# Optimization experiments

Measured on AMD Instinct MI355X. Metric: run time of the kernel, lower is better.

The kernel has to match this reference:

```python
import jax, jax.numpy as jnp
import numpy as np

N_NODES = 100000
N_EDGES = 1600000
IN_DIM, HID_DIM, OUT_DIM = 128, 64, 40


def setup_inputs() -> dict:
    key = jax.random.key(0)
    k1, k2, k3, k4, k5, k6 = jax.random.split(key, 6)
    x = jax.random.normal(k1, (N_NODES, IN_DIM), dtype=jnp.float32)
    edge_index = jax.random.randint(k2, (2, N_EDGES), 0, N_NODES, dtype=jnp.int64)
    W1 = jax.random.normal(k3, (IN_DIM, HID_DIM), dtype=jnp.float32) * 0.05
    b1 = jnp.zeros((HID_DIM,), dtype=jnp.float32)
    W2 = jax.random.normal(k4, (HID_DIM, OUT_DIM), dtype=jnp.float32) * 0.05
    b2 = jnp.zeros((OUT_DIM,), dtype=jnp.float32)
    return {"x": x, "edge_index": edge_index, "W1": W1, "b1": b1, "W2": W2, "b2": b2}


def gcn_conv(x, src, dst, W, b, n_nodes):
    """PyG GCNConv: linear -> symmetric-normalized aggregation (with self loops) -> + bias."""
    h = x @ W                                                # [N, C_out]
    # degree of targets, including the implicit self loop (weight 1 each)
    deg = jax.ops.segment_sum(jnp.ones_like(dst, dtype=h.dtype), dst,
                              num_segments=n_nodes) + 1.0    # [N]
    dinv = jax.lax.rsqrt(deg)                                # deg >= 1, always valid
    norm = dinv[src] * dinv[dst]                             # [E] edge norm coefficients
    msg = h[src] * norm[:, None]                             # [E, C_out] gather + scale
    agg = jax.ops.segment_sum(msg, dst, num_segments=n_nodes)
    # self-loop contribution: norm_ii = dinv_i * dinv_i
    agg = agg + h * (dinv * dinv)[:, None]
    return agg + b


def reference(x, edge_index, W1, b1, W2, b2):
    src, dst = edge_index[0], edge_index[1]  # source_to_target flow (PyG default)
    n = x.shape[0]
    h = gcn_conv(x, src, dst, W1, b1, n)
    h = jax.nn.relu(h)
    # dropout is identity in eval mode (training=False)
    out = gcn_conv(h, src, dst, W2, b2, n)
    return out
```

## Files before the change

kernel.cpp:

```cpp
#include <hip/hip_runtime.h>
#include <math.h>

#define N_NODES 100000
#define N_EDGES 1600000
#define IN_DIM 128
#define HID_DIM 64
#define OUT_DIM 40

#define NPAD 102400

#define BUCKET_SHIFT 7
#define BUCKET_NODES 128
#define N_BUCKETS 782
#define CHUNK 2048
#define N_CHUNKS 784

typedef _Float16 f16;
typedef _Float16 f16x2 __attribute__((ext_vector_type(2)));
typedef _Float16 f16x4 __attribute__((ext_vector_type(4)));
typedef _Float16 f16x8 __attribute__((ext_vector_type(8)));
typedef float f32x4 __attribute__((ext_vector_type(4)));


__global__ __launch_bounds__(256) void hist_kernel(const int* __restrict__ dst,
                                                   int* __restrict__ hist) {
    __shared__ int lh[N_BUCKETS];
    int c = blockIdx.x;
    int t = threadIdx.x;
    for (int b = t; b < N_BUCKETS; b += 256) lh[b] = 0;
    __syncthreads();
    int e0 = c * CHUNK;
    for (int i = t; i < CHUNK; i += 256) {
        int e = e0 + i;
        if (e < N_EDGES) atomicAdd(&lh[dst[e] >> BUCKET_SHIFT], 1);
    }
    __syncthreads();
    for (int b = t; b < N_BUCKETS; b += 256) hist[c * N_BUCKETS + b] = lh[b];
}

__global__ __launch_bounds__(256) void scan_chunks_kernel(const int* __restrict__ hist,
                                                          int* __restrict__ base,
                                                          int* __restrict__ bucketTotal) {
    __shared__ int lds[256];
    int b = blockIdx.x;
    int t = threadIdx.x;
    int v[4];
    int s = 0;
    for (int k = 0; k < 4; ++k) {
        int c = 4 * t + k;
        int cv = (c < N_CHUNKS) ? hist[c * N_BUCKETS + b] : 0;
        v[k] = s;
        s += cv;
    }
    lds[t] = s;
    __syncthreads();
    for (int off = 1; off < 256; off <<= 1) {
        int val = (t >= off) ? lds[t - off] : 0;
        __syncthreads();
        lds[t] += val;
        __syncthreads();
    }
    int excl = (t == 0) ? 0 : lds[t - 1];
    for (int k = 0; k < 4; ++k) {
        int c = 4 * t + k;
        if (c < N_CHUNKS) base[b * N_CHUNKS + c] = excl + v[k];
    }
    if (t == 255) bucketTotal[b] = lds[255];
}

__global__ __launch_bounds__(256) void scan_buckets_kernel(const int* __restrict__ bucketTotal,
                                                           int* __restrict__ bucketBase) {
    __shared__ int lds[256];
    int t = threadIdx.x;
    int v[4];
    int s = 0;
    for (int k = 0; k < 4; ++k) {
        int b = 4 * t + k;
        int cv = (b < N_BUCKETS) ? bucketTotal[b] : 0;
        v[k] = s;
        s += cv;
    }
    lds[t] = s;
    __syncthreads();
    for (int off = 1; off < 256; off <<= 1) {
        int val = (t >= off) ? lds[t - off] : 0;
        __syncthreads();
        lds[t] += val;
        __syncthreads();
    }
    int excl = (t == 0) ? 0 : lds[t - 1];
    for (int k = 0; k < 4; ++k) {
        int b = 4 * t + k;
        if (b < N_BUCKETS) bucketBase[b] = excl + v[k];
    }
}

__global__ __launch_bounds__(256) void scatter_kernel(const int* __restrict__ src,
                                                      const int* __restrict__ dst,
                                                      const int* __restrict__ base,
                                                      const int* __restrict__ bucketBase,
                                                      int* __restrict__ stage) {
    __shared__ int lbase[N_BUCKETS];
    __shared__ int lcnt[N_BUCKETS];
    int bid = blockIdx.x;
    int chunk = (bid & 7) * 98 + (bid >> 3);
    int t = threadIdx.x;
    for (int b = t; b < N_BUCKETS; b += 256) {
        lbase[b] = base[b * N_CHUNKS + chunk] + bucketBase[b];
        lcnt[b] = 0;
    }
    __syncthreads();
    int e0 = chunk * CHUNK;
    for (int i = t; i < CHUNK; i += 256) {
        int e = e0 + i;
        if (e < N_EDGES) {
            int d = dst[e];
            int b = d >> BUCKET_SHIFT;
            int pos = lbase[b] + atomicAdd(&lcnt[b], 1);
            stage[pos] = ((d & (BUCKET_NODES - 1)) << 17) | src[e];
        }
    }
}

__global__ __launch_bounds__(256) void place_kernel(const int* __restrict__ stage,
                                                    const int* __restrict__ bucketBase,
                                                    int* __restrict__ csr,
                                                    int* __restrict__ row_start,
                                                    int* __restrict__ cnt,
                                                    float* __restrict__ dinv) {
    __shared__ int lhist[BUCKET_NODES];
    __shared__ int lscan[BUCKET_NODES];
    __shared__ int lstart[BUCKET_NODES];
    __shared__ int lcur[BUCKET_NODES];
    int b = blockIdx.x;
    int t = threadIdx.x;
    int est = bucketBase[b];
    int een = (b == N_BUCKETS - 1) ? N_EDGES : bucketBase[b + 1];
    if (t < BUCKET_NODES) { lhist[t] = 0; lcur[t] = 0; }
    __syncthreads();
    for (int e = est + t; e < een; e += 256) atomicAdd(&lhist[stage[e] >> 17], 1);
    __syncthreads();
    if (t < BUCKET_NODES) lscan[t] = lhist[t];
    __syncthreads();
    for (int off = 1; off < BUCKET_NODES; off <<= 1) {
        int val = (t >= off && t < BUCKET_NODES) ? lscan[t - off] : 0;
        __syncthreads();
        if (t < BUCKET_NODES) lscan[t] += val;
        __syncthreads();
    }
    if (t < BUCKET_NODES) {
        int myexcl = (t == 0) ? 0 : lscan[t - 1];
        lstart[t] = est + myexcl;
        int node = (b << BUCKET_SHIFT) + t;
        if (node < N_NODES) {
            row_start[node] = est + myexcl;
            cnt[node] = lhist[t];
            dinv[node] = rsqrtf((float)lhist[t] + 1.0f);
        }
    }
    __syncthreads();
    for (int e = est + t; e < een; e += 256) {
        int rec = stage[e];
        int dl = rec >> 17;
        int pos = lstart[dl] + atomicAdd(&lcur[dl], 1);
        csr[pos] = rec & 0x1FFFF;
    }
}

__global__ __launch_bounds__(256) void w1frag_kernel(const float* __restrict__ W1,
                                                     f16* __restrict__ w1f) {
    int g = blockIdx.x * 256 + threadIdx.x;
    int f = g >> 6, L = g & 63;
    int s = f >> 2, c = f & 3;
    int q = L >> 4, n = L & 15;
    f16x8 v;
#pragma unroll
    for (int j = 0; j < 8; ++j) {
        int k = 32 * s + 8 * q + j;
        v[j] = (f16)W1[k * HID_DIM + 16 * c + n];
    }
    *(f16x8*)&w1f[(size_t)g * 8] = v;
}

__global__ __launch_bounds__(256) void gemm1_kernel(const float* __restrict__ x,
                                                    const f16* __restrict__ w1f,
                                                    const float* __restrict__ dinv,
                                                    f16* __restrict__ h1p) {
    __shared__ f16 aT[1088 * 8];
    int t = threadIdx.x;
    int nodeBase = blockIdx.x * 64;
    int L = t & 63;

    const f16x8* w1f8 = (const f16x8*)w1f;
    f16x8 bfrag[16];
#pragma unroll
    for (int f = 0; f < 16; ++f) bfrag[f] = w1f8[f * 64 + L];

#pragma unroll
    for (int i = 0; i < 8; ++i) {
        int idx = i * 256 + t;
        int node = idx >> 5;
        int col4 = idx & 31;
        int gnode = nodeBase + node;
        if (gnode >= N_NODES) gnode = N_NODES - 1;
        float4 v = *(const float4*)&x[(size_t)gnode * IN_DIM + col4 * 4];
        int w = node >> 4, m = node & 15;
        int s = col4 >> 3, q = (col4 >> 1) & 3, j0 = (col4 & 1) * 4;
        f16x4 h;
        h.x = (f16)v.x; h.y = (f16)v.y; h.z = (f16)v.z; h.w = (f16)v.w;
        int idx16 = (w * 4 + s) * 68 + 17 * q + m;
        *(f16x4*)&aT[idx16 * 8 + j0] = h;
    }
    __syncthreads();

    int wv = t >> 6;
    int q = L >> 4, m = L & 15;
    f32x4 acc[4] = {};
#pragma unroll
    for (int s = 0; s < 4; ++s) {
        f16x8 afrag = *(const f16x8*)&aT[((wv * 4 + s) * 68 + 17 * q + m) * 8];
#pragma unroll
        for (int c = 0; c < 4; ++c)
            acc[c] = __builtin_amdgcn_mfma_f32_16x16x32_f16(afrag, bfrag[s * 4 + c], acc[c], 0, 0, 0);
    }

#pragma unroll
    for (int r = 0; r < 4; ++r) {
        int node = nodeBase + 16 * wv + q * 4 + r;
        if (node < N_NODES) {
            float di = dinv[node];
#pragma unroll
            for (int c = 0; c < 4; ++c)
                h1p[(size_t)node * HID_DIM + 16 * c + m] = (f16)(acc[c][r] * di);
        }
    }
}

__global__ __launch_bounds__(256) void agg1_kernel(const f16* __restrict__ h1p,
                                                   const int* __restrict__ csr,
                                                   const int* __restrict__ row_start,
                                                   const int* __restrict__ cnt,
                                                   const float* __restrict__ dinv,
                                                   const float* __restrict__ b1,
                                                   float* __restrict__ z) {
    int node = blockIdx.x * 8 + (threadIdx.x >> 5);
    int lane = threadIdx.x & 31;
    if (node >= N_NODES) return;
    const f16x2* h = (const f16x2*)h1p;
    float2 acc;
    {
        f16x2 sv = h[(size_t)node * 32 + lane];
        acc.x = (float)sv.x;
        acc.y = (float)sv.y;
    }
    int n = cnt[node];
    const int* cp = csr + row_start[node];
    int k = 0;
    if (n >= 4) {
        int i0 = cp[0], i1 = cp[1], i2 = cp[2], i3 = cp[3];
        for (; k + 8 <= n; k += 4) {
            int j0 = cp[k + 4], j1 = cp[k + 5], j2 = cp[k + 6], j3 = cp[k + 7];
            f16x2 f0 = h[(size_t)i0 * 32 + lane];
            f16x2 f1 = h[(size_t)i1 * 32 + lane];
            f16x2 f2 = h[(size_t)i2 * 32 + lane];
            f16x2 f3 = h[(size_t)i3 * 32 + lane];
            acc.x += (float)f0.x + (float)f1.x + (float)f2.x + (float)f3.x;
            acc.y += (float)f0.y + (float)f1.y + (float)f2.y + (float)f3.y;
            i0 = j0; i1 = j1; i2 = j2; i3 = j3;
        }
        {
            f16x2 f0 = h[(size_t)i0 * 32 + lane];
            f16x2 f1 = h[(size_t)i1 * 32 + lane];
            f16x2 f2 = h[(size_t)i2 * 32 + lane];
            f16x2 f3 = h[(size_t)i3 * 32 + lane];
            acc.x += (float)f0.x + (float)f1.x + (float)f2.x + (float)f3.x;
            acc.y += (float)f0.y + (float)f1.y + (float)f2.y + (float)f3.y;
            k += 4;
        }
    }
    for (; k < n; ++k) {
        f16x2 f = h[(size_t)cp[k] * 32 + lane];
        acc.x += (float)f.x;
        acc.y += (float)f.y;
    }
    float di = dinv[node];
    float2 bb = *(const float2*)&b1[2 * lane];
    float v0 = acc.x * di + bb.x;
    float v1 = acc.y * di + bb.y;
    float2 o;
    o.x = v0 > 0.f ? v0 : 0.f;
    o.y = v1 > 0.f ? v1 : 0.f;
    *(float2*)&z[(size_t)node * HID_DIM + 2 * lane] = o;
}

#define G2_ZS 68
__global__ __launch_bounds__(256) void gemm2_kernel(const float* __restrict__ z,
                                                    const float* __restrict__ W2,
                                                    const float* __restrict__ dinv,
                                                    f16* __restrict__ h2p) {
    __shared__ float ws[HID_DIM * OUT_DIM];
    __shared__ float zT[HID_DIM * G2_ZS];
    int t = threadIdx.x;
    int nodeBase = blockIdx.x * 64;

    const float4* W4 = (const float4*)W2;
    float4* ws4 = (float4*)ws;
    for (int i = t; i < (HID_DIM * OUT_DIM) / 4; i += 256) ws4[i] = W4[i];

    int kg = t & 31;
    int nd = t >> 5;
#pragma unroll
    for (int m = 0; m < 8; ++m) {
        int node = nd + 8 * m;
        int n = nodeBase + node;
        float v0 = 0.f, v1 = 0.f;
        if (n < N_NODES) {
            const float* zr = z + (size_t)n * HID_DIM;
            v0 = zr[kg];
            v1 = zr[kg + 32];
        }
        zT[kg * G2_ZS + node] = v0;
        zT[(kg + 32) * G2_ZS + node] = v1;
    }
    __syncthreads();

    int g = t >> 4;
    int c = t & 15;
    if (c < 10) {
        float acc[4][4] = {};
#pragma unroll 4
        for (int k = 0; k < HID_DIM; ++k) {
            float4 zv = *(const float4*)&zT[k * G2_ZS + 4 * g];
            float4 wv = *(const float4*)&ws[k * OUT_DIM + 4 * c];
            acc[0][0] += zv.x * wv.x; acc[0][1] += zv.x * wv.y; acc[0][2] += zv.x * wv.z; acc[0][3] += zv.x * wv.w;
            acc[1][0] += zv.y * wv.x; acc[1][1] += zv.y * wv.y; acc[1][2] += zv.y * wv.z; acc[1][3] += zv.y * wv.w;
            acc[2][0] += zv.z * wv.x; acc[2][1] += zv.z * wv.y; acc[2][2] += zv.z * wv.z; acc[2][3] += zv.z * wv.w;
            acc[3][0] += zv.w * wv.x; acc[3][1] += zv.w * wv.y; acc[3][2] += zv.w * wv.z; acc[3][3] += zv.w * wv.w;
        }
#pragma unroll
        for (int i = 0; i < 4; ++i) {
            int n = nodeBase + 4 * g + i;
            if (n < N_NODES) {
                float di = dinv[n];
                f16x4 o;
                o.x = (f16)(acc[i][0] * di);
                o.y = (f16)(acc[i][1] * di);
                o.z = (f16)(acc[i][2] * di);
                o.w = (f16)(acc[i][3] * di);
                *(f16x4*)&h2p[(size_t)n * OUT_DIM + 4 * c] = o;
            }
        }
    }
}

__global__ __launch_bounds__(256) void agg2_kernel(const f16* __restrict__ h2p,
                                                   const int* __restrict__ csr,
                                                   const int* __restrict__ row_start,
                                                   const int* __restrict__ cnt,
                                                   const float* __restrict__ dinv,
                                                   const float* __restrict__ b2,
                                                   float* __restrict__ out) {
    int node = blockIdx.x * 8 + (threadIdx.x >> 5);
    int lane = threadIdx.x & 31;
    if (node >= N_NODES || lane >= 20) return;
    const f16x2* h = (const f16x2*)h2p;
    float2 acc;
    {
        f16x2 sv = h[(size_t)node * 20 + lane];
        acc.x = (float)sv.x;
        acc.y = (float)sv.y;
    }
    int n = cnt[node];
    const int* cp = csr + row_start[node];
    int k = 0;
    if (n >= 4) {
        int i0 = cp[0], i1 = cp[1], i2 = cp[2], i3 = cp[3];
        for (; k + 8 <= n; k += 4) {
            int j0 = cp[k + 4], j1 = cp[k + 5], j2 = cp[k + 6], j3 = cp[k + 7];
            f16x2 f0 = h[(size_t)i0 * 20 + lane];
            f16x2 f1 = h[(size_t)i1 * 20 + lane];
            f16x2 f2 = h[(size_t)i2 * 20 + lane];
            f16x2 f3 = h[(size_t)i3 * 20 + lane];
            acc.x += (float)f0.x + (float)f1.x + (float)f2.x + (float)f3.x;
            acc.y += (float)f0.y + (float)f1.y + (float)f2.y + (float)f3.y;
            i0 = j0; i1 = j1; i2 = j2; i3 = j3;
        }
        {
            f16x2 f0 = h[(size_t)i0 * 20 + lane];
            f16x2 f1 = h[(size_t)i1 * 20 + lane];
            f16x2 f2 = h[(size_t)i2 * 20 + lane];
            f16x2 f3 = h[(size_t)i3 * 20 + lane];
            acc.x += (float)f0.x + (float)f1.x + (float)f2.x + (float)f3.x;
            acc.y += (float)f0.y + (float)f1.y + (float)f2.y + (float)f3.y;
            k += 4;
        }
    }
    for (; k < n; ++k) {
        f16x2 f = h[(size_t)cp[k] * 20 + lane];
        acc.x += (float)f.x;
        acc.y += (float)f.y;
    }
    float di = dinv[node];
    float2 bb = *(const float2*)&b2[2 * lane];
    float2 o;
    o.x = acc.x * di + bb.x;
    o.y = acc.y * di + bb.y;
    *(float2*)&out[(size_t)node * OUT_DIM + 2 * lane] = o;
}

extern "C" void kernel_launch(void* const* d_in, const int* in_sizes, int n_in,
                              void* d_out, int out_size, void* d_ws, size_t ws_size,
                              hipStream_t stream) {
    const float* x  = (const float*)d_in[0];
    const int*   ei = (const int*)d_in[1];
    const float* W1 = (const float*)d_in[2];
    const float* b1 = (const float*)d_in[3];
    const float* W2 = (const float*)d_in[4];
    const float* b2 = (const float*)d_in[5];
    float* out = (float*)d_out;

    const int* src = ei;
    const int* dst = ei + N_EDGES;

    int* wsi        = (int*)d_ws;
    int* hist       = wsi;
    int* base       = hist + N_CHUNKS * N_BUCKETS;
    int* bucketTotal= base + N_BUCKETS * N_CHUNKS;
    int* bucketBase = bucketTotal + 1024;
    int* row_start  = bucketBase + 1024;
    int* cnt        = row_start + NPAD;
    int* csr        = cnt + NPAD;
    int* stage      = csr + N_EDGES;
    float* dinv     = (float*)(stage + N_EDGES);
    float* z        = dinv + NPAD;
    f16*   h1p      = (f16*)(z + (size_t)N_NODES * HID_DIM);
    f16*   h2p      = h1p + (size_t)N_NODES * HID_DIM;
    f16*   w1f      = h2p + (size_t)N_NODES * OUT_DIM;

    hist_kernel<<<N_CHUNKS, 256, 0, stream>>>(dst, hist);
    scan_chunks_kernel<<<N_BUCKETS, 256, 0, stream>>>(hist, base, bucketTotal);
    scan_buckets_kernel<<<1, 256, 0, stream>>>(bucketTotal, bucketBase);
    scatter_kernel<<<N_CHUNKS, 256, 0, stream>>>(src, dst, base, bucketBase, stage);
    place_kernel<<<N_BUCKETS, 256, 0, stream>>>(stage, bucketBase, csr, row_start, cnt, dinv);

    w1frag_kernel<<<4, 256, 0, stream>>>(W1, w1f);
    gemm1_kernel<<<(N_NODES + 63) / 64, 256, 0, stream>>>(x, w1f, dinv, h1p);
    agg1_kernel<<<(N_NODES + 7) / 8, 256, 0, stream>>>(h1p, csr, row_start, cnt, dinv, b1, z);
    gemm2_kernel<<<(N_NODES + 63) / 64, 256, 0, stream>>>(z, W2, dinv, h2p);
    agg2_kernel<<<(N_NODES + 7) / 8, 256, 0, stream>>>(h2p, csr, row_start, cnt, dinv, b2, out);
}
```

Baseline: 239.6 us.

## Fuse layer-1 aggregation with layer-2 GEMM using MFMA on fp16 tile

New measurement: 226.5 us. -5.5%, faster.

```diff
diff --git a/kernel.cpp b/kernel.cpp
--- a/kernel.cpp
+++ b/kernel.cpp
@@ -167,19 +167,31 @@
     }
 }
 
-__global__ __launch_bounds__(256) void w1frag_kernel(const float* __restrict__ W1,
-                                                     f16* __restrict__ w1f) {
+__global__ __launch_bounds__(256) void wfrag_kernel(const float* __restrict__ W1,
+                                                    const float* __restrict__ W2,
+                                                    f16* __restrict__ w1f,
+                                                    f16* __restrict__ w2f) {
     int g = blockIdx.x * 256 + threadIdx.x;
-    int f = g >> 6, L = g & 63;
-    int s = f >> 2, c = f & 3;
-    int q = L >> 4, n = L & 15;
-    f16x8 v;
-#pragma unroll
-    for (int j = 0; j < 8; ++j) {
-        int k = 32 * s + 8 * q + j;
-        v[j] = (f16)W1[k * HID_DIM + 16 * c + n];
-    }
-    *(f16x8*)&w1f[(size_t)g * 8] = v;
+    if (g < 1024) {
+        int f = g >> 6, L = g & 63;
+        int s = f >> 2, c = f & 3;
+        int q = L >> 4, n = L & 15;
+        f16x8 v;
+#pragma unroll
+        for (int j = 0; j < 8; ++j) v[j] = (f16)W1[(32 * s + 8 * q + j) * HID_DIM + 16 * c + n];
+        *(f16x8*)&w1f[(size_t)g * 8] = v;
+    } else if (g < 1024 + 384) {
+        int gg = g - 1024;
+        int f = gg >> 6, L = gg & 63;
+        int s = f / 3, c = f % 3;
+        int q = L >> 4, n = L & 15;
+        int col = 16 * c + n;
+        f16x8 v;
+#pragma unroll
+        for (int j = 0; j < 8; ++j)
+            v[j] = (col < OUT_DIM) ? (f16)W2[(32 * s + 8 * q + j) * OUT_DIM + col] : (f16)0.f;
+        *(f16x8*)&w2f[(size_t)gg * 8] = v;
+    }
 }
 
 __global__ __launch_bounds__(256) void gemm1_kernel(const float* __restrict__ x,
@@ -236,119 +248,96 @@
     }
 }
 
-__global__ __launch_bounds__(256) void agg1_kernel(const f16* __restrict__ h1p,
-                                                   const int* __restrict__ csr,
-                                                   const int* __restrict__ row_start,
-                                                   const int* __restrict__ cnt,
-                                                   const float* __restrict__ dinv,
-                                                   const float* __restrict__ b1,
-                                                   float* __restrict__ z) {
-    int node = blockIdx.x * 8 + (threadIdx.x >> 5);
-    int lane = threadIdx.x & 31;
-    if (node >= N_NODES) return;
+#define ZSTR 72
+__global__ __launch_bounds__(256) void agg1mm_kernel(const f16* __restrict__ h1p,
+                                                     const int* __restrict__ csr,
+                                                     const int* __restrict__ row_start,
+                                                     const int* __restrict__ cnt,
+                                                     const float* __restrict__ dinv,
+                                                     const float* __restrict__ b1,
+                                                     const f16* __restrict__ w2f,
+                                                     f16* __restrict__ h2p) {
+    __shared__ f16 zT[64 * ZSTR];
+    int t = threadIdx.x;
+    int nodeBase = blockIdx.x * 64;
+    int halfw = t >> 5;
+    int lane = t & 31;
     const f16x2* h = (const f16x2*)h1p;
-    float2 acc;
-    {
-        f16x2 sv = h[(size_t)node * 32 + lane];
-        acc.x = (float)sv.x;
-        acc.y = (float)sv.y;
-    }
-    int n = cnt[node];
-    const int* cp = csr + row_start[node];
-    int k = 0;
-    if (n >= 4) {
-        int i0 = cp[0], i1 = cp[1], i2 = cp[2], i3 = cp[3];
-        for (; k + 8 <= n; k += 4) {
-            int j0 = cp[k + 4], j1 = cp[k + 5], j2 = cp[k + 6], j3 = cp[k + 7];
-            f16x2 f0 = h[(size_t)i0 * 32 + lane];
-            f16x2 f1 = h[(size_t)i1 * 32 + lane];
-            f16x2 f2 = h[(size_t)i2 * 32 + lane];
-            f16x2 f3 = h[(size_t)i3 * 32 + lane];
-            acc.x += (float)f0.x + (float)f1.x + (float)f2.x + (float)f3.x;
-            acc.y += (float)f0.y + (float)f1.y + (float)f2.y + (float)f3.y;
-            i0 = j0; i1 = j1; i2 = j2; i3 = j3;
-        }
-        {
-            f16x2 f0 = h[(size_t)i0 * 32 + lane];
-            f16x2 f1 = h[(size_t)i1 * 32 + lane];
-            f16x2 f2 = h[(size_t)i2 * 32 + lane];
-            f16x2 f3 = h[(size_t)i3 * 32 + lane];
-            acc.x += (float)f0.x + (float)f1.x + (float)f2.x + (float)f3.x;
-            acc.y += (float)f0.y + (float)f1.y + (float)f2.y + (float)f3.y;
-            k += 4;
-        }
-    }
-    for (; k < n; ++k) {
-        f16x2 f = h[(size_t)cp[k] * 32 + lane];
-        acc.x += (float)f.x;
-        acc.y += (float)f.y;
-    }
-    float di = dinv[node];
     float2 bb = *(const float2*)&b1[2 * lane];
-    float v0 = acc.x * di + bb.x;
-    float v1 = acc.y * di + bb.y;
-    float2 o;
-    o.x = v0 > 0.f ? v0 : 0.f;
-    o.y = v1 > 0.f ? v1 : 0.f;
-    *(float2*)&z[(size_t)node * HID_DIM + 2 * lane] = o;
-}
-
-#define G2_ZS 68
-__global__ __launch_bounds__(256) void gemm2_kernel(const float* __restrict__ z,
-                                                    const float* __restrict__ W2,
-                                                    const float* __restrict__ dinv,
-                                                    f16* __restrict__ h2p) {
-    __shared__ float ws[HID_DIM * OUT_DIM];
-    __shared__ float zT[HID_DIM * G2_ZS];
-    int t = threadIdx.x;
-    int nodeBase = blockIdx.x * 64;
-
-    const float4* W4 = (const float4*)W2;
-    float4* ws4 = (float4*)ws;
-    for (int i = t; i < (HID_DIM * OUT_DIM) / 4; i += 256) ws4[i] = W4[i];
-
-    int kg = t & 31;
-    int nd = t >> 5;
-#pragma unroll
-    for (int m = 0; m < 8; ++m) {
-        int node = nd + 8 * m;
-        int n = nodeBase + node;
-        float v0 = 0.f, v1 = 0.f;
-        if (n < N_NODES) {
-            const float* zr = z + (size_t)n * HID_DIM;
-            v0 = zr[kg];
-            v1 = zr[kg + 32];
-        }
-        zT[kg * G2_ZS + node] = v0;
-        zT[(kg + 32) * G2_ZS + node] = v1;
-    }
-    __syncthreads();
-
-    int g = t >> 4;
-    int c = t & 15;
-    if (c < 10) {
-        float acc[4][4] = {};
-#pragma unroll 4
-        for (int k = 0; k < HID_DIM; ++k) {
-            float4 zv = *(const float4*)&zT[k * G2_ZS + 4 * g];
-            float4 wv = *(const float4*)&ws[k * OUT_DIM + 4 * c];
-            acc[0][0] += zv.x * wv.x; acc[0][1] += zv.x * wv.y; acc[0][2] += zv.x * wv.z; acc[0][3] += zv.x * wv.w;
-            acc[1][0] += zv.y * wv.x; acc[1][1] += zv.y * wv.y; acc[1][2] += zv.y * wv.z; acc[1][3] += zv.y * wv.w;
-            acc[2][0] += zv.z * wv.x; acc[2][1] += zv.z * wv.y; acc[2][2] += zv.z * wv.z; acc[2][3] += zv.z * wv.w;
-            acc[3][0] += zv.w * wv.x; acc[3][1] += zv.w * wv.y; acc[3][2] += zv.w * wv.z; acc[3][3] += zv.w * wv.w;
-        }
-#pragma unroll
-        for (int i = 0; i < 4; ++i) {
-            int n = nodeBase + 4 * g + i;
-            if (n < N_NODES) {
-                float di = dinv[n];
-                f16x4 o;
-                o.x = (f16)(acc[i][0] * di);
-                o.y = (f16)(acc[i][1] * di);
-                o.z = (f16)(acc[i][2] * di);
-                o.w = (f16)(acc[i][3] * di);
-                *(f16x4*)&h2p[(size_t)n * OUT_DIM + 4 * c] = o;
+
+    for (int r = 0; r < 8; ++r) {
+        int nodeLocal = r * 8 + halfw;
+        int node = nodeBase + nodeLocal;
+        float2 acc;
+        acc.x = 0.f; acc.y = 0.f;
+        if (node < N_NODES) {
+            f16x2 sv = h[(size_t)node * 32 + lane];
+            acc.x = (float)sv.x;
+            acc.y = (float)sv.y;
+            int n = cnt[node];
+            const int* cp = csr + row_start[node];
+            int k = 0;
+            if (n >= 4) {
+                int i0 = cp[0], i1 = cp[1], i2 = cp[2], i3 = cp[3];
+                for (; k + 8 <= n; k += 4) {
+                    int j0 = cp[k + 4], j1 = cp[k + 5], j2 = cp[k + 6], j3 = cp[k + 7];
+                    f16x2 f0 = h[(size_t)i0 * 32 + lane];
+                    f16x2 f1 = h[(size_t)i1 * 32 + lane];
+                    f16x2 f2 = h[(size_t)i2 * 32 + lane];
+                    f16x2 f3 = h[(size_t)i3 * 32 + lane];
+                    acc.x += (float)f0.x + (float)f1.x + (float)f2.x + (float)f3.x;
+                    acc.y += (float)f0.y + (float)f1.y + (float)f2.y + (float)f3.y;
+                    i0 = j0; i1 = j1; i2 = j2; i3 = j3;
+                }
+                {
+                    f16x2 f0 = h[(size_t)i0 * 32 + lane];
+                    f16x2 f1 = h[(size_t)i1 * 32 + lane];
+                    f16x2 f2 = h[(size_t)i2 * 32 + lane];
+                    f16x2 f3 = h[(size_t)i3 * 32 + lane];
+                    acc.x += (float)f0.x + (float)f1.x + (float)f2.x + (float)f3.x;
+                    acc.y += (float)f0.y + (float)f1.y + (float)f2.y + (float)f3.y;
+                    k += 4;
+                }
             }
+            for (; k < n; ++k) {
+                f16x2 f = h[(size_t)cp[k] * 32 + lane];
+                acc.x += (float)f.x;
+                acc.y += (float)f.y;
+            }
+            float di = dinv[node];
+            float v0 = acc.x * di + bb.x;
+            float v1 = acc.y * di + bb.y;
+            acc.x = v0 > 0.f ? v0 : 0.f;
+            acc.y = v1 > 0.f ? v1 : 0.f;
+        }
+        f16x2 o;
+        o.x = (f16)acc.x;
+        o.y = (f16)acc.y;
+        *(f16x2*)&zT[nodeLocal * ZSTR + 2 * lane] = o;
+    }
+    __syncthreads();
+
+    int wv = t >> 6;
+    int L = t & 63;
+    int q = L >> 4, m = L & 15;
+    const f16x8* w2f8 = (const f16x8*)w2f;
+    f32x4 acc2[3] = {};
+#pragma unroll
+    for (int s = 0; s < 2; ++s) {
+        f16x8 afrag = *(const f16x8*)&zT[(16 * wv + m) * ZSTR + 32 * s + 8 * q];
+#pragma unroll
+        for (int c = 0; c < 3; ++c)
+            acc2[c] = __builtin_amdgcn_mfma_f32_16x16x32_f16(afrag, w2f8[(s * 3 + c) * 64 + L], acc2[c], 0, 0, 0);
+    }
+#pragma unroll
+    for (int r = 0; r < 4; ++r) {
+        int node = nodeBase + 16 * wv + q * 4 + r;
+        if (node < N_NODES) {
+            float di = dinv[node];
+            h2p[(size_t)node * OUT_DIM + m]      = (f16)(acc2[0][r] * di);
+            h2p[(size_t)node * OUT_DIM + 16 + m] = (f16)(acc2[1][r] * di);
+            if (m < 8)
+                h2p[(size_t)node * OUT_DIM + 32 + m] = (f16)(acc2[2][r] * di);
         }
     }
 }
@@ -432,10 +421,10 @@
     int* csr        = cnt + NPAD;
     int* stage      = csr + N_EDGES;
     float* dinv     = (float*)(stage + N_EDGES);
-    float* z        = dinv + NPAD;
-    f16*   h1p      = (f16*)(z + (size_t)N_NODES * HID_DIM);
+    f16*   h1p      = (f16*)(dinv + NPAD);
     f16*   h2p      = h1p + (size_t)N_NODES * HID_DIM;
     f16*   w1f      = h2p + (size_t)N_NODES * OUT_DIM;
+    f16*   w2f      = w1f + 8192;
 
     hist_kernel<<<N_CHUNKS, 256, 0, stream>>>(dst, hist);
     scan_chunks_kernel<<<N_BUCKETS, 256, 0, stream>>>(hist, base, bucketTotal);
@@ -443,9 +432,8 @@
     scatter_kernel<<<N_CHUNKS, 256, 0, stream>>>(src, dst, base, bucketBase, stage);
     place_kernel<<<N_BUCKETS, 256, 0, stream>>>(stage, bucketBase, csr, row_start, cnt, dinv);
 
-    w1frag_kernel<<<4, 256, 0, stream>>>(W1, w1f);
+    wfrag_kernel<<<6, 256, 0, stream>>>(W1, W2, w1f, w2f);
     gemm1_kernel<<<(N_NODES + 63) / 64, 256, 0, stream>>>(x, w1f, dinv, h1p);
-    agg1_kernel<<<(N_NODES + 7) / 8, 256, 0, stream>>>(h1p, csr, row_start, cnt, dinv, b1, z);
-    gemm2_kernel<<<(N_NODES + 63) / 64, 256, 0, stream>>>(z, W2, dinv, h2p);
+    agg1mm_kernel<<<(N_NODES + 63) / 64, 256, 0, stream>>>(h1p, csr, row_start, cnt, dinv, b1, w2f, h2p);
     agg2_kernel<<<(N_NODES + 7) / 8, 256, 0, stream>>>(h2p, csr, row_start, cnt, dinv, b2, out);
 }
```
